# Optimization experiments

Measured on AMD Instinct MI355X. Metric: run time of the kernel, lower is better.

Reference implementation:

```python
import jax, jax.numpy as jnp
import numpy as np

DIM = 192
HEADS = 6
HEAD_DIM = DIM // HEADS  # 32
N = 64                   # prod(window_size) = 4*4*4
BW = 4096                # num_windows * B
NEG = -1e9               # finite stand-in for -inf additive mask


def setup_inputs() -> dict:
    key = jax.random.key(0)
    k_x, k_m, k_qkv, k_p, k_pb = jax.random.split(key, 5)
    x = jax.random.normal(k_x, (BW, N, N and 192))  # (BW, N, C)
    x = jax.random.normal(k_x, (BW, N, DIM), dtype=jnp.float32)
    # Shifted-window style additive mask: block-diagonal groups of tokens.
    # Each window gets a random group id per token; tokens attend only within
    # their group (0), cross-group gets NEG. Diagonal always allowed.
    gid = jax.random.randint(k_m, (BW, N), 0, 3)  # (BW, N) group ids in {0,1,2}
    same = gid[:, :, None] == gid[:, None, :]     # (BW, N, N) bool
    mask = jnp.where(same, 0.0, NEG).astype(jnp.float32)[:, None, :, :]  # (BW,1,N,N)
    w_qkv = jax.random.normal(k_qkv, (3 * DIM, DIM), dtype=jnp.float32) * (DIM ** -0.5)
    w_proj = jax.random.normal(k_p, (DIM, DIM), dtype=jnp.float32) * (DIM ** -0.5)
    b_proj = jax.random.normal(k_pb, (DIM,), dtype=jnp.float32) * 0.02
    return {"x": x, "mask": mask, "w_qkv": w_qkv, "w_proj": w_proj, "b_proj": b_proj}


def reference(x, mask, w_qkv, w_proj, b_proj):
    b, n, c = x.shape
    scale = HEAD_DIM ** -0.5
    # qkv linear (no bias) then split: 'b n (three heads c) -> three b heads n c'
    qkv = jnp.einsum('bnc,dc->bnd', x, w_qkv)               # (b, n, 3*C)
    qkv = qkv.reshape(b, n, 3, HEADS, HEAD_DIM)
    qkv = jnp.transpose(qkv, (2, 0, 3, 1, 4))               # (3, b, heads, n, hd)
    q, k, v = qkv[0], qkv[1], qkv[2]
    q = q * scale
    # scaled_dot_product_attention with additive mask (scale=1 since q pre-scaled)
    scores = jnp.einsum('bhqd,bhkd->bhqk', q, k) + mask     # (b, heads, n, n)
    probs = jax.nn.softmax(scores, axis=-1)
    out = jnp.einsum('bhqk,bhkd->bhqd', probs, v)           # (b, heads, n, hd)
    # 'b k n c -> b n (k c)'
    out = jnp.transpose(out, (0, 2, 1, 3)).reshape(b, n, c)
    # output projection (bias=True in nn.Linear default)
    return jnp.einsum('bnc,dc->bnd', out, w_proj) + b_proj
```

## Files before the change

kernel.cpp:

```cpp
#include <hip/hip_runtime.h>

#define NTOK 64
#define DIM 192
#define HEADS 6
#define HD 32

typedef __attribute__((ext_vector_type(8))) short short8;
typedef __attribute__((ext_vector_type(4))) float floatx4;

__device__ __forceinline__ short f2bf(float f) {
    union { float f; unsigned int u; } c; c.f = f;
    unsigned int r = (c.u + 0x7FFFu + ((c.u >> 16) & 1u)) >> 16;
    return (short)(unsigned short)r;
}

__device__ __forceinline__ unsigned pkbf(float a, float b) {
    unsigned ua = __float_as_uint(a) + 0x8000u;
    unsigned ub = __float_as_uint(b) + 0x8000u;
    return __builtin_amdgcn_perm(ub, ua, 0x07060302u);
}
__device__ __forceinline__ short8 cvt8(const float* p) {
    const float4* v = reinterpret_cast<const float4*>(p);
    float4 lo = v[0], hi = v[1];
    union { unsigned u[4]; short8 s; } r;
    r.u[0] = pkbf(lo.x, lo.y);
    r.u[1] = pkbf(lo.z, lo.w);
    r.u[2] = pkbf(hi.x, hi.y);
    r.u[3] = pkbf(hi.z, hi.w);
    return r.s;
}

#define RS  200
#define VTS 68
#define PSS 68

__global__ __launch_bounds__(256, 2)
void wattn_fused(const float* __restrict__ x, const float* __restrict__ mask,
                 const float* __restrict__ wqkv, const float* __restrict__ wproj,
                 const float* __restrict__ bproj, float* __restrict__ out) {
    __shared__ short qs [NTOK * RS];
    __shared__ short ksm[NTOK * RS];
    __shared__ short vsT[DIM  * VTS];

    const int bw   = blockIdx.x;
    const int tid  = (int)threadIdx.x;
    const int wave = tid >> 6;
    const int lane = tid & 63;
    const int r    = lane & 15;
    const int quad = lane >> 4;

    const float* xb = x + (size_t)bw * (NTOK * DIM);

    short8 a[4][6];
    #pragma unroll
    for (int mt = 0; mt < 4; ++mt) {
        #pragma unroll
        for (int s = 0; s < 6; ++s)
            a[mt][s] = cvt8(xb + (mt * 16 + r) * DIM + s * 32 + quad * 8);
    }

    const int W0 = wave * 144;
    #pragma unroll
    for (int nt = 0; nt < 9; ++nt) {
        const int d0 = W0 + nt * 16;
        floatx4 acc[4];
        #pragma unroll
        for (int mt = 0; mt < 4; ++mt) acc[mt] = (floatx4){0.f, 0.f, 0.f, 0.f};
        #pragma unroll
        for (int s = 0; s < 6; ++s) {
            short8 b = cvt8(wqkv + (d0 + r) * DIM + s * 32 + quad * 8);
            #pragma unroll
            for (int mt = 0; mt < 4; ++mt)
                acc[mt] = __builtin_amdgcn_mfma_f32_16x16x32_bf16(a[mt][s], b, acc[mt], 0, 0, 0);
        }
        if (d0 < DIM) {
            const int dc = d0 + r;
            #pragma unroll
            for (int mt = 0; mt < 4; ++mt) {
                #pragma unroll
                for (int g = 0; g < 4; ++g)
                    qs[(mt * 16 + quad * 4 + g) * RS + dc] =
                        f2bf(acc[mt][g] * 0.17677669529663688f);
            }
        } else if (d0 < 2 * DIM) {
            const int dc = d0 - DIM + r;
            #pragma unroll
            for (int mt = 0; mt < 4; ++mt) {
                #pragma unroll
                for (int g = 0; g < 4; ++g)
                    ksm[(mt * 16 + quad * 4 + g) * RS + dc] = f2bf(acc[mt][g]);
            }
        } else {
            const int dc = d0 - 2 * DIM + r;
            #pragma unroll
            for (int mt = 0; mt < 4; ++mt) {
                #pragma unroll
                for (int g = 0; g < 4; ++g)
                    vsT[dc * VTS + (mt * 16 + quad * 4 + g)] = f2bf(acc[mt][g]);
            }
        }
    }
    __syncthreads();

    const float* mb = mask + (size_t)bw * (NTOK * NTOK);
    short* pw = qs + wave * (32 * PSS);
    float oreg[3][2][2][4];

    short8 aq[3][2];
    #pragma unroll
    for (int i = 0; i < 3; ++i) {
        const int uu = wave * 3 + i, h = uu >> 1, half = uu & 1;
        #pragma unroll
        for (int mt = 0; mt < 2; ++mt)
            aq[i][mt] = *reinterpret_cast<const short8*>(
                qs + (half * 32 + mt * 16 + r) * RS + h * HD + quad * 8);
    }
    __syncthreads();

    #pragma unroll
    for (int i = 0; i < 3; ++i) {
        const int uu   = wave * 3 + i;
        const int h    = uu >> 1;
        const int half = uu & 1;
        const int hc   = h * HD;

        short8 bk[4];
        #pragma unroll
        for (int nt = 0; nt < 4; ++nt)
            bk[nt] = *reinterpret_cast<const short8*>(
                ksm + (nt * 16 + r) * RS + hc + quad * 8);

        floatx4 sa[2][4];
        #pragma unroll
        for (int mt = 0; mt < 2; ++mt) {
            #pragma unroll
            for (int nt = 0; nt < 4; ++nt) {
                floatx4 z = (floatx4){0.f, 0.f, 0.f, 0.f};
                sa[mt][nt] = __builtin_amdgcn_mfma_f32_16x16x32_bf16(aq[i][mt], bk[nt], z, 0, 0, 0);
            }
        }

        #pragma unroll
        for (int mt = 0; mt < 2; ++mt) {
            #pragma unroll
            for (int g = 0; g < 4; ++g) {
                const int qt = half * 32 + mt * 16 + quad * 4 + g;
                #pragma unroll
                for (int nt = 0; nt < 4; ++nt)
                    sa[mt][nt][g] += mb[qt * NTOK + nt * 16 + r];
            }
        }

        float rs_[2][4];
        #pragma unroll
        for (int mt = 0; mt < 2; ++mt) {
            #pragma unroll
            for (int g = 0; g < 4; ++g) {
                float m = fmaxf(fmaxf(sa[mt][0][g], sa[mt][1][g]),
                                fmaxf(sa[mt][2][g], sa[mt][3][g]));
                m = fmaxf(m, __shfl_xor(m, 1));
                m = fmaxf(m, __shfl_xor(m, 2));
                m = fmaxf(m, __shfl_xor(m, 4));
                m = fmaxf(m, __shfl_xor(m, 8));
                float sum = 0.f;
                #pragma unroll
                for (int nt = 0; nt < 4; ++nt) {
                    float p = __expf(sa[mt][nt][g] - m);
                    sa[mt][nt][g] = p;
                    sum += p;
                }
                sum += __shfl_xor(sum, 1);
                sum += __shfl_xor(sum, 2);
                sum += __shfl_xor(sum, 4);
                sum += __shfl_xor(sum, 8);
                rs_[mt][g] = sum;
            }
        }

        #pragma unroll
        for (int mt = 0; mt < 2; ++mt) {
            #pragma unroll
            for (int g = 0; g < 4; ++g) {
                #pragma unroll
                for (int nt = 0; nt < 4; ++nt)
                    pw[(mt * 16 + quad * 4 + g) * PSS + nt * 16 + r] = f2bf(sa[mt][nt][g]);
            }
        }

        floatx4 oa[2][2];
        #pragma unroll
        for (int mt = 0; mt < 2; ++mt) {
            #pragma unroll
            for (int nv = 0; nv < 2; ++nv) oa[mt][nv] = (floatx4){0.f, 0.f, 0.f, 0.f};
        }
        #pragma unroll
        for (int kk = 0; kk < 2; ++kk) {
            short8 bv[2], ap[2];
            #pragma unroll
            for (int nv = 0; nv < 2; ++nv)
                bv[nv] = *reinterpret_cast<const short8*>(
                    vsT + (hc + nv * 16 + r) * VTS + kk * 32 + quad * 8);
            #pragma unroll
            for (int mt = 0; mt < 2; ++mt)
                ap[mt] = *reinterpret_cast<const short8*>(
                    pw + (mt * 16 + r) * PSS + kk * 32 + quad * 8);
            #pragma unroll
            for (int mt = 0; mt < 2; ++mt) {
                #pragma unroll
                for (int nv = 0; nv < 2; ++nv)
                    oa[mt][nv] = __builtin_amdgcn_mfma_f32_16x16x32_bf16(ap[mt], bv[nv], oa[mt][nv], 0, 0, 0);
            }
        }
        #pragma unroll
        for (int mt = 0; mt < 2; ++mt) {
            #pragma unroll
            for (int nv = 0; nv < 2; ++nv) {
                #pragma unroll
                for (int g = 0; g < 4; ++g)
                    oreg[i][mt][nv][g] = oa[mt][nv][g] / rs_[mt][g];
            }
        }
    }

    __syncthreads();

    #pragma unroll
    for (int i = 0; i < 3; ++i) {
        const int uu = wave * 3 + i, h = uu >> 1, half = uu & 1;
        #pragma unroll
        for (int mt = 0; mt < 2; ++mt) {
            #pragma unroll
            for (int nv = 0; nv < 2; ++nv) {
                #pragma unroll
                for (int g = 0; g < 4; ++g)
                    qs[(half * 32 + mt * 16 + quad * 4 + g) * RS + h * HD + nv * 16 + r] =
                        f2bf(oreg[i][mt][nv][g]);
            }
        }
    }
    __syncthreads();

    short8 ao[4][6];
    #pragma unroll
    for (int mt = 0; mt < 4; ++mt) {
        #pragma unroll
        for (int s = 0; s < 6; ++s)
            ao[mt][s] = *reinterpret_cast<const short8*>(
                qs + (mt * 16 + r) * RS + s * 32 + quad * 8);
    }

    float* ob = out + (size_t)bw * (NTOK * DIM);
    const int D0 = wave * 48;
    #pragma unroll
    for (int nt = 0; nt < 3; ++nt) {
        const int d0 = D0 + nt * 16;
        const float bias = bproj[d0 + r];
        floatx4 acc[4];
        #pragma unroll
        for (int mt = 0; mt < 4; ++mt) acc[mt] = (floatx4){bias, bias, bias, bias};
        #pragma unroll
        for (int s = 0; s < 6; ++s) {
            short8 b = cvt8(wproj + (d0 + r) * DIM + s * 32 + quad * 8);
            #pragma unroll
            for (int mt = 0; mt < 4; ++mt)
                acc[mt] = __builtin_amdgcn_mfma_f32_16x16x32_bf16(ao[mt][s], b, acc[mt], 0, 0, 0);
        }
        #pragma unroll
        for (int mt = 0; mt < 4; ++mt) {
            #pragma unroll
            for (int g = 0; g < 4; ++g)
                ob[(mt * 16 + quad * 4 + g) * DIM + d0 + r] = acc[mt][g];
        }
    }
}

extern "C" void kernel_launch(void* const* d_in, const int* in_sizes, int n_in,
                              void* d_out, int out_size, void* d_ws, size_t ws_size,
                              hipStream_t stream) {
    const float* x    = (const float*)d_in[0];
    const float* mask = (const float*)d_in[1];
    const float* wqkv = (const float*)d_in[2];
    const float* wp   = (const float*)d_in[3];
    const float* bp   = (const float*)d_in[4];
    float* out = (float*)d_out;
    const int nblocks = in_sizes[0] / (NTOK * DIM);
    wattn_fused<<<nblocks, 256, 0, stream>>>(x, mask, wqkv, wp, bp, out);
}
```

Measured before the change: 673.2 us.

## Pre-convert weights to bf16, keep Q and P in registers, transpose MFMA outputs

Adds a prep kernel that converts the QKV and projection weights to bf16 once per launch, folding the softmax scale into the Q rows, and stores them in workspace. The fused kernel then loads bf16 weights directly instead of converting them per block. Q is computed per head in registers and rearranged with lane shuffles instead of going through shared memory. Softmax probabilities are likewise shuffled into MFMA operands instead of being staged in LDS, which frees the Q buffer and raises occupancy to 3 blocks. Outputs and bias are written as float4 through transposed MFMA operand order. The cost is an extra kernel launch and recomputing Q per head slice, with more register pressure.

```diff
diff --git a/kernel.cpp b/kernel.cpp
--- a/kernel.cpp
+++ b/kernel.cpp
@@ -2,11 +2,16 @@
 
 #define NTOK 64
 #define DIM 192
-#define HEADS 6
 #define HD 32
+
+#define RS  200
+#define VTS 68
+#define WQN (576 * DIM)
+#define WPN (DIM * DIM)
 
 typedef __attribute__((ext_vector_type(8))) short short8;
 typedef __attribute__((ext_vector_type(4))) float floatx4;
+typedef __attribute__((ext_vector_type(2))) unsigned int uint2v;
 
 __device__ __forceinline__ short f2bf(float f) {
     union { float f; unsigned int u; } c; c.f = f;
@@ -15,10 +20,11 @@
 }
 
 __device__ __forceinline__ unsigned pkbf(float a, float b) {
-    unsigned ua = __float_as_uint(a) + 0x8000u;
-    unsigned ub = __float_as_uint(b) + 0x8000u;
+    unsigned ua = __float_as_uint(a); ua += 0x7FFFu + ((ua >> 16) & 1u);
+    unsigned ub = __float_as_uint(b); ub += 0x7FFFu + ((ub >> 16) & 1u);
     return __builtin_amdgcn_perm(ub, ua, 0x07060302u);
 }
+
 __device__ __forceinline__ short8 cvt8(const float* p) {
     const float4* v = reinterpret_cast<const float4*>(p);
     float4 lo = v[0], hi = v[1];
@@ -30,223 +36,273 @@
     return r.s;
 }
 
-#define RS  200
-#define VTS 68
-#define PSS 68
-
-__global__ __launch_bounds__(256, 2)
+__device__ __forceinline__ short8 qshuf(floatx4 v0, floatx4 v1, int lane) {
+    const int q = lane >> 4;
+    const unsigned p0a = pkbf(v0[0], v0[1]);
+    const unsigned p0b = pkbf(v0[2], v0[3]);
+    const unsigned p1a = pkbf(v1[0], v1[1]);
+    const unsigned p1b = pkbf(v1[2], v1[3]);
+    const int s0 = (lane & 15) | ((q & 1) << 5);
+    const int s1 = s0 + 16;
+    const unsigned l0 = (unsigned)__shfl((int)p0a, s0);
+    const unsigned h0 = (unsigned)__shfl((int)p1a, s0);
+    const unsigned l1 = (unsigned)__shfl((int)p0b, s0);
+    const unsigned h1 = (unsigned)__shfl((int)p1b, s0);
+    const unsigned l2 = (unsigned)__shfl((int)p0a, s1);
+    const unsigned h2 = (unsigned)__shfl((int)p1a, s1);
+    const unsigned l3 = (unsigned)__shfl((int)p0b, s1);
+    const unsigned h3 = (unsigned)__shfl((int)p1b, s1);
+    const bool hi = q >= 2;
+    union { unsigned u[4]; short8 s; } ret;
+    ret.u[0] = hi ? h0 : l0;
+    ret.u[1] = hi ? h1 : l1;
+    ret.u[2] = hi ? h2 : l2;
+    ret.u[3] = hi ? h3 : l3;
+    return ret.s;
+}
+
+__global__ void wprep(const float* __restrict__ wqkv, const float* __restrict__ wproj,
+                      short* __restrict__ wqb, short* __restrict__ wpb) {
+    const int i = blockIdx.x * 256 + (int)threadIdx.x;
+    for (int e = i; e < WQN; e += 192 * 256) {
+        float v = wqkv[e];
+        if (e < DIM * DIM) v *= 0.17677669529663688f;
+        wqb[e] = f2bf(v);
+    }
+    for (int e = i; e < WPN; e += 192 * 256) wpb[e] = f2bf(wproj[e]);
+}
+
+template <int WS>
+__global__ __launch_bounds__(256, 3)
 void wattn_fused(const float* __restrict__ x, const float* __restrict__ mask,
                  const float* __restrict__ wqkv, const float* __restrict__ wproj,
-                 const float* __restrict__ bproj, float* __restrict__ out) {
-    __shared__ short qs [NTOK * RS];
+                 const float* __restrict__ bproj, float* __restrict__ out,
+                 const short* __restrict__ wqb, const short* __restrict__ wpb) {
     __shared__ short ksm[NTOK * RS];
-    __shared__ short vsT[DIM  * VTS];
+    __shared__ short vsT[DIM * VTS];
 
     const int bw   = blockIdx.x;
     const int tid  = (int)threadIdx.x;
     const int wave = tid >> 6;
     const int lane = tid & 63;
     const int r    = lane & 15;
-    const int quad = lane >> 4;
+    const int q    = lane >> 4;
 
     const float* xb = x + (size_t)bw * (NTOK * DIM);
 
+    auto ldq = [&](int off) -> short8 {
+        if constexpr (WS) return *reinterpret_cast<const short8*>(wqb + off);
+        else              return cvt8(wqkv + off);
+    };
+    auto ldp = [&](int off) -> short8 {
+        if constexpr (WS) return *reinterpret_cast<const short8*>(wpb + off);
+        else              return cvt8(wproj + off);
+    };
+
     short8 a[4][6];
     #pragma unroll
     for (int mt = 0; mt < 4; ++mt) {
         #pragma unroll
         for (int s = 0; s < 6; ++s)
-            a[mt][s] = cvt8(xb + (mt * 16 + r) * DIM + s * 32 + quad * 8);
-    }
-
-    const int W0 = wave * 144;
-    #pragma unroll
-    for (int nt = 0; nt < 9; ++nt) {
-        const int d0 = W0 + nt * 16;
-        floatx4 acc[4];
-        #pragma unroll
-        for (int mt = 0; mt < 4; ++mt) acc[mt] = (floatx4){0.f, 0.f, 0.f, 0.f};
-        #pragma unroll
-        for (int s = 0; s < 6; ++s) {
-            short8 b = cvt8(wqkv + (d0 + r) * DIM + s * 32 + quad * 8);
-            #pragma unroll
-            for (int mt = 0; mt < 4; ++mt)
-                acc[mt] = __builtin_amdgcn_mfma_f32_16x16x32_bf16(a[mt][s], b, acc[mt], 0, 0, 0);
-        }
-        if (d0 < DIM) {
-            const int dc = d0 + r;
+            a[mt][s] = cvt8(xb + (mt * 16 + r) * DIM + s * 32 + q * 8);
+    }
+
+    if (wave < 2) {
+        const int cb = wave * 96;
+        #pragma unroll
+        for (int nt = 0; nt < 6; ++nt) {
+            const int dk = cb + nt * 16;
+            floatx4 acc[4];
+            #pragma unroll
+            for (int mt = 0; mt < 4; ++mt) acc[mt] = (floatx4){0.f, 0.f, 0.f, 0.f};
+            #pragma unroll
+            for (int s = 0; s < 6; ++s) {
+                const short8 b8 = ldq((DIM + dk + r) * DIM + s * 32 + q * 8);
+                #pragma unroll
+                for (int mt = 0; mt < 4; ++mt)
+                    acc[mt] = __builtin_amdgcn_mfma_f32_16x16x32_bf16(b8, a[mt][s], acc[mt], 0, 0, 0);
+            }
             #pragma unroll
             for (int mt = 0; mt < 4; ++mt) {
-                #pragma unroll
-                for (int g = 0; g < 4; ++g)
-                    qs[(mt * 16 + quad * 4 + g) * RS + dc] =
-                        f2bf(acc[mt][g] * 0.17677669529663688f);
-            }
-        } else if (d0 < 2 * DIM) {
-            const int dc = d0 - DIM + r;
+                uint2v u;
+                u.x = pkbf(acc[mt][0], acc[mt][1]);
+                u.y = pkbf(acc[mt][2], acc[mt][3]);
+                *reinterpret_cast<uint2v*>(ksm + (mt * 16 + r) * RS + dk + q * 4) = u;
+            }
+        }
+    } else {
+        const int cb = (wave - 2) * 96;
+        #pragma unroll
+        for (int nt = 0; nt < 6; ++nt) {
+            const int dv = cb + nt * 16;
+            floatx4 acc[4];
+            #pragma unroll
+            for (int mt = 0; mt < 4; ++mt) acc[mt] = (floatx4){0.f, 0.f, 0.f, 0.f};
+            #pragma unroll
+            for (int s = 0; s < 6; ++s) {
+                const short8 b8 = ldq((2 * DIM + dv + r) * DIM + s * 32 + q * 8);
+                #pragma unroll
+                for (int mt = 0; mt < 4; ++mt)
+                    acc[mt] = __builtin_amdgcn_mfma_f32_16x16x32_bf16(a[mt][s], b8, acc[mt], 0, 0, 0);
+            }
             #pragma unroll
             for (int mt = 0; mt < 4; ++mt) {
-                #pragma unroll
-                for (int g = 0; g < 4; ++g)
-                    ksm[(mt * 16 + quad * 4 + g) * RS + dc] = f2bf(acc[mt][g]);
-            }
-        } else {
-            const int dc = d0 - 2 * DIM + r;
-            #pragma unroll
-            for (int mt = 0; mt < 4; ++mt) {
-                #pragma unroll
-                for (int g = 0; g < 4; ++g)
-                    vsT[dc * VTS + (mt * 16 + quad * 4 + g)] = f2bf(acc[mt][g]);
-            }
-        }
-    }
-    __syncthreads();
-
-    const float* mb = mask + (size_t)bw * (NTOK * NTOK);
-    short* pw = qs + wave * (32 * PSS);
-    float oreg[3][2][2][4];
-
-    short8 aq[3][2];
+                uint2v u;
+                u.x = pkbf(acc[mt][0], acc[mt][1]);
+                u.y = pkbf(acc[mt][2], acc[mt][3]);
+                *reinterpret_cast<uint2v*>(vsT + (dv + r) * VTS + mt * 16 + q * 4) = u;
+            }
+        }
+    }
+
+    short8 bq[3][2];
     #pragma unroll
     for (int i = 0; i < 3; ++i) {
         const int uu = wave * 3 + i, h = uu >> 1, half = uu & 1;
-        #pragma unroll
-        for (int mt = 0; mt < 2; ++mt)
-            aq[i][mt] = *reinterpret_cast<const short8*>(
-                qs + (half * 32 + mt * 16 + r) * RS + h * HD + quad * 8);
+        floatx4 qa[2][2];
+        #pragma unroll
+        for (int dt = 0; dt < 2; ++dt) {
+            #pragma unroll
+            for (int qt = 0; qt < 2; ++qt) qa[dt][qt] = (floatx4){0.f, 0.f, 0.f, 0.f};
+        }
+        #pragma unroll
+        for (int s = 0; s < 6; ++s) {
+            const short8 w0 = ldq((h * HD + r) * DIM + s * 32 + q * 8);
+            const short8 w1 = ldq((h * HD + 16 + r) * DIM + s * 32 + q * 8);
+            #pragma unroll
+            for (int qt = 0; qt < 2; ++qt) {
+                qa[0][qt] = __builtin_amdgcn_mfma_f32_16x16x32_bf16(w0, a[half * 2 + qt][s], qa[0][qt], 0, 0, 0);
+                qa[1][qt] = __builtin_amdgcn_mfma_f32_16x16x32_bf16(w1, a[half * 2 + qt][s], qa[1][qt], 0, 0, 0);
+            }
+        }
+        if constexpr (!WS) {
+            #pragma unroll
+            for (int dt = 0; dt < 2; ++dt)
+                #pragma unroll
+                for (int qt = 0; qt < 2; ++qt)
+                    #pragma unroll
+                    for (int g = 0; g < 4; ++g)
+                        qa[dt][qt][g] *= 0.17677669529663688f;
+        }
+        bq[i][0] = qshuf(qa[0][0], qa[1][0], lane);
+        bq[i][1] = qshuf(qa[0][1], qa[1][1], lane);
     }
     __syncthreads();
 
-    #pragma unroll
-    for (int i = 0; i < 3; ++i) {
-        const int uu   = wave * 3 + i;
-        const int h    = uu >> 1;
-        const int half = uu & 1;
-        const int hc   = h * HD;
-
-        short8 bk[4];
-        #pragma unroll
-        for (int nt = 0; nt < 4; ++nt)
-            bk[nt] = *reinterpret_cast<const short8*>(
-                ksm + (nt * 16 + r) * RS + hc + quad * 8);
-
-        floatx4 sa[2][4];
-        #pragma unroll
-        for (int mt = 0; mt < 2; ++mt) {
-            #pragma unroll
-            for (int nt = 0; nt < 4; ++nt) {
-                floatx4 z = (floatx4){0.f, 0.f, 0.f, 0.f};
-                sa[mt][nt] = __builtin_amdgcn_mfma_f32_16x16x32_bf16(aq[i][mt], bk[nt], z, 0, 0, 0);
-            }
-        }
-
-        #pragma unroll
-        for (int mt = 0; mt < 2; ++mt) {
-            #pragma unroll
-            for (int g = 0; g < 4; ++g) {
-                const int qt = half * 32 + mt * 16 + quad * 4 + g;
-                #pragma unroll
-                for (int nt = 0; nt < 4; ++nt)
-                    sa[mt][nt][g] += mb[qt * NTOK + nt * 16 + r];
-            }
-        }
-
-        float rs_[2][4];
-        #pragma unroll
-        for (int mt = 0; mt < 2; ++mt) {
-            #pragma unroll
-            for (int g = 0; g < 4; ++g) {
-                float m = fmaxf(fmaxf(sa[mt][0][g], sa[mt][1][g]),
-                                fmaxf(sa[mt][2][g], sa[mt][3][g]));
-                m = fmaxf(m, __shfl_xor(m, 1));
-                m = fmaxf(m, __shfl_xor(m, 2));
-                m = fmaxf(m, __shfl_xor(m, 4));
-                m = fmaxf(m, __shfl_xor(m, 8));
-                float sum = 0.f;
-                #pragma unroll
-                for (int nt = 0; nt < 4; ++nt) {
-                    float p = __expf(sa[mt][nt][g] - m);
-                    sa[mt][nt][g] = p;
-                    sum += p;
-                }
-                sum += __shfl_xor(sum, 1);
-                sum += __shfl_xor(sum, 2);
-                sum += __shfl_xor(sum, 4);
-                sum += __shfl_xor(sum, 8);
-                rs_[mt][g] = sum;
-            }
-        }
-
-        #pragma unroll
-        for (int mt = 0; mt < 2; ++mt) {
-            #pragma unroll
-            for (int g = 0; g < 4; ++g) {
-                #pragma unroll
-                for (int nt = 0; nt < 4; ++nt)
-                    pw[(mt * 16 + quad * 4 + g) * PSS + nt * 16 + r] = f2bf(sa[mt][nt][g]);
-            }
-        }
-
-        floatx4 oa[2][2];
-        #pragma unroll
-        for (int mt = 0; mt < 2; ++mt) {
-            #pragma unroll
-            for (int nv = 0; nv < 2; ++nv) oa[mt][nv] = (floatx4){0.f, 0.f, 0.f, 0.f};
-        }
-        #pragma unroll
-        for (int kk = 0; kk < 2; ++kk) {
-            short8 bv[2], ap[2];
-            #pragma unroll
-            for (int nv = 0; nv < 2; ++nv)
-                bv[nv] = *reinterpret_cast<const short8*>(
-                    vsT + (hc + nv * 16 + r) * VTS + kk * 32 + quad * 8);
-            #pragma unroll
-            for (int mt = 0; mt < 2; ++mt)
-                ap[mt] = *reinterpret_cast<const short8*>(
-                    pw + (mt * 16 + r) * PSS + kk * 32 + quad * 8);
-            #pragma unroll
-            for (int mt = 0; mt < 2; ++mt) {
-                #pragma unroll
-                for (int nv = 0; nv < 2; ++nv)
-                    oa[mt][nv] = __builtin_amdgcn_mfma_f32_16x16x32_bf16(ap[mt], bv[nv], oa[mt][nv], 0, 0, 0);
-            }
-        }
-        #pragma unroll
-        for (int mt = 0; mt < 2; ++mt) {
-            #pragma unroll
-            for (int nv = 0; nv < 2; ++nv) {
-                #pragma unroll
-                for (int g = 0; g < 4; ++g)
-                    oreg[i][mt][nv][g] = oa[mt][nv][g] / rs_[mt][g];
-            }
-        }
-    }
-
-    __syncthreads();
+    const float* mb  = mask + (size_t)bw * (NTOK * NTOK);
+    const float* mbl = mb + 256 * q + r;
+    uint2v obf[3][2][2];
 
     #pragma unroll
     for (int i = 0; i < 3; ++i) {
         const int uu = wave * 3 + i, h = uu >> 1, half = uu & 1;
-        #pragma unroll
-        for (int mt = 0; mt < 2; ++mt) {
+
+        float mv[2][4][4];
+        #pragma unroll
+        for (int qt = 0; qt < 2; ++qt)
+            #pragma unroll
+            for (int kt = 0; kt < 4; ++kt)
+                #pragma unroll
+                for (int g = 0; g < 4; ++g)
+                    mv[qt][kt][g] = mbl[kt * 1024 + g * 64 + half * 32 + qt * 16];
+
+        short8 bk[4];
+        #pragma unroll
+        for (int kt = 0; kt < 4; ++kt)
+            bk[kt] = *reinterpret_cast<const short8*>(ksm + (kt * 16 + r) * RS + h * HD + q * 8);
+
+        floatx4 sa[4][2];
+        #pragma unroll
+        for (int kt = 0; kt < 4; ++kt) {
+            #pragma unroll
+            for (int qt = 0; qt < 2; ++qt) {
+                floatx4 z = (floatx4){0.f, 0.f, 0.f, 0.f};
+                sa[kt][qt] = __builtin_amdgcn_mfma_f32_16x16x32_bf16(bk[kt], bq[i][qt], z, 0, 0, 0);
+            }
+        }
+        #pragma unroll
+        for (int kt = 0; kt < 4; ++kt)
+            #pragma unroll
+            for (int qt = 0; qt < 2; ++qt)
+                #pragma unroll
+                for (int g = 0; g < 4; ++g)
+                    sa[kt][qt][g] += mv[qt][kt][g];
+
+        float rinv[2];
+        #pragma unroll
+        for (int qt = 0; qt < 2; ++qt) {
+            float mx = sa[0][qt][0];
+            #pragma unroll
+            for (int kt = 0; kt < 4; ++kt)
+                #pragma unroll
+                for (int g = 0; g < 4; ++g) mx = fmaxf(mx, sa[kt][qt][g]);
+            mx = fmaxf(mx, __shfl_xor(mx, 16));
+            mx = fmaxf(mx, __shfl_xor(mx, 32));
+            float sm = 0.f;
+            #pragma unroll
+            for (int kt = 0; kt < 4; ++kt) {
+                #pragma unroll
+                for (int g = 0; g < 4; ++g) {
+                    float p = __expf(sa[kt][qt][g] - mx);
+                    sa[kt][qt][g] = p;
+                    sm += p;
+                }
+            }
+            sm += __shfl_xor(sm, 16);
+            sm += __shfl_xor(sm, 32);
+            rinv[qt] = 1.0f / sm;
+        }
+
+        short8 ap[2][2];
+        #pragma unroll
+        for (int qt = 0; qt < 2; ++qt) {
+            #pragma unroll
+            for (int kk = 0; kk < 2; ++kk)
+                ap[qt][kk] = qshuf(sa[2 * kk][qt], sa[2 * kk + 1][qt], lane);
+        }
+
+        short8 bv[2][2];
+        #pragma unroll
+        for (int nv = 0; nv < 2; ++nv)
+            #pragma unroll
+            for (int kk = 0; kk < 2; ++kk)
+                bv[nv][kk] = *reinterpret_cast<const short8*>(
+                    vsT + (h * HD + nv * 16 + r) * VTS + kk * 32 + q * 8);
+
+        #pragma unroll
+        for (int qt = 0; qt < 2; ++qt) {
             #pragma unroll
             for (int nv = 0; nv < 2; ++nv) {
-                #pragma unroll
-                for (int g = 0; g < 4; ++g)
-                    qs[(half * 32 + mt * 16 + quad * 4 + g) * RS + h * HD + nv * 16 + r] =
-                        f2bf(oreg[i][mt][nv][g]);
-            }
-        }
-    }
+                floatx4 o = (floatx4){0.f, 0.f, 0.f, 0.f};
+                o = __builtin_amdgcn_mfma_f32_16x16x32_bf16(bv[nv][0], ap[qt][0], o, 0, 0, 0);
+                o = __builtin_amdgcn_mfma_f32_16x16x32_bf16(bv[nv][1], ap[qt][1], o, 0, 0, 0);
+                uint2v u;
+                u.x = pkbf(o[0] * rinv[qt], o[1] * rinv[qt]);
+                u.y = pkbf(o[2] * rinv[qt], o[3] * rinv[qt]);
+                obf[i][qt][nv] = u;
+            }
+        }
+    }
+
     __syncthreads();
+    #pragma unroll
+    for (int i = 0; i < 3; ++i) {
+        const int uu = wave * 3 + i, h = uu >> 1, half = uu & 1;
+        #pragma unroll
+        for (int qt = 0; qt < 2; ++qt)
+            #pragma unroll
+            for (int nv = 0; nv < 2; ++nv)
+                *reinterpret_cast<uint2v*>(
+                    ksm + (half * 32 + qt * 16 + r) * RS + h * HD + nv * 16 + q * 4) = obf[i][qt][nv];
+    }
+    __syncthreads();
 
     short8 ao[4][6];
     #pragma unroll
     for (int mt = 0; mt < 4; ++mt) {
         #pragma unroll
         for (int s = 0; s < 6; ++s)
-            ao[mt][s] = *reinterpret_cast<const short8*>(
-                qs + (mt * 16 + r) * RS + s * 32 + quad * 8);
+            ao[mt][s] = *reinterpret_cast<const short8*>(ksm + (mt * 16 + r) * RS + s * 32 + q * 8);
     }
 
     float* ob = out + (size_t)bw * (NTOK * DIM);
@@ -254,22 +310,22 @@
     #pragma unroll
     for (int nt = 0; nt < 3; ++nt) {
         const int d0 = D0 + nt * 16;
-        const float bias = bproj[d0 + r];
+        const float4 b4 = *reinterpret_cast<const float4*>(bproj + d0 + q * 4);
         floatx4 acc[4];
         #pragma unroll
-        for (int mt = 0; mt < 4; ++mt) acc[mt] = (floatx4){bias, bias, bias, bias};
+        for (int mt = 0; mt < 4; ++mt) acc[mt] = (floatx4){b4.x, b4.y, b4.z, b4.w};
         #pragma unroll
         for (int s = 0; s < 6; ++s) {
-            short8 b = cvt8(wproj + (d0 + r) * DIM + s * 32 + quad * 8);
+            const short8 w8 = ldp((d0 + r) * DIM + s * 32 + q * 8);
             #pragma unroll
             for (int mt = 0; mt < 4; ++mt)
-                acc[mt] = __builtin_amdgcn_mfma_f32_16x16x32_bf16(ao[mt][s], b, acc[mt], 0, 0, 0);
+                acc[mt] = __builtin_amdgcn_mfma_f32_16x16x32_bf16(w8, ao[mt][s], acc[mt], 0, 0, 0);
         }
         #pragma unroll
         for (int mt = 0; mt < 4; ++mt) {
-            #pragma unroll
-            for (int g = 0; g < 4; ++g)
-                ob[(mt * 16 + quad * 4 + g) * DIM + d0 + r] = acc[mt][g];
+            float4 st;
+            st.x = acc[mt][0]; st.y = acc[mt][1]; st.z = acc[mt][2]; st.w = acc[mt][3];
+            *reinterpret_cast<float4*>(ob + (mt * 16 + r) * DIM + d0 + q * 4) = st;
         }
     }
 }
@@ -284,5 +340,13 @@
     const float* bp   = (const float*)d_in[4];
     float* out = (float*)d_out;
     const int nblocks = in_sizes[0] / (NTOK * DIM);
-    wattn_fused<<<nblocks, 256, 0, stream>>>(x, mask, wqkv, wp, bp, out);
-}
+    const size_t need = (size_t)(WQN + WPN) * sizeof(short);
+    if (d_ws != nullptr && ws_size >= need) {
+        short* wqb = (short*)d_ws;
+        short* wpb = wqb + WQN;
+        wprep<<<192, 256, 0, stream>>>(wqkv, wp, wqb, wpb);
+        wattn_fused<1><<<nblocks, 256, 0, stream>>>(x, mask, wqkv, wp, bp, out, wqb, wpb);
+    } else {
+        wattn_fused<0><<<nblocks, 256, 0, stream>>>(x, mask, wqkv, wp, bp, out, nullptr, nullptr);
+    }
+}
```

New measurement: 976.4 us. 45.0% more time.
